# Performance work log

Hardware: AMD Instinct MI355X
Metric: run time of the kernel (lower is better)

The kernel has to match this reference:

```python
import jax, jax.numpy as jnp
import numpy as np

B, S, D, H = 2, 2048, 1024, 16
HD = D // H
NEG = -9000000000000000.0


def setup_inputs() -> dict:
    key = jax.random.key(0)
    ks = jax.random.split(key, 12)
    scale = 1.0 / np.sqrt(D)
    inp = {
        "k": jax.random.normal(ks[0], (B, S, D), jnp.float32),
        "q": jax.random.normal(ks[1], (B, S, D), jnp.float32),
        "v": jax.random.normal(ks[2], (B, S, D), jnp.float32),
        # causal mask, float (0/1), shape [B, 1, S, S] as expected by __call__
        "mask": jnp.broadcast_to(jnp.tril(jnp.ones((S, S), jnp.float32))[None, None], (B, 1, S, S)),
        "Wq": jax.random.normal(ks[3], (D, D), jnp.float32) * scale,
        "bq": jnp.zeros((D,), jnp.float32),
        "Wk": jax.random.normal(ks[4], (D, D), jnp.float32) * scale,
        "bk": jnp.zeros((D,), jnp.float32),
        "Wv": jax.random.normal(ks[5], (D, D), jnp.float32) * scale,
        "bv": jnp.zeros((D,), jnp.float32),
        "Wo": jax.random.normal(ks[6], (D, D), jnp.float32) * scale,
        "bo": jnp.zeros((D,), jnp.float32),
    }
    return inp


def _split_heads(x):
    # [B, S, D] -> [B, H, S, HD]
    return x.reshape(B, S, H, HD).transpose(0, 2, 1, 3)


def reference(k, q, v, mask, Wq, bq, Wk, bk, Wv, bv, Wo, bo):
    keys = _split_heads(k @ Wk + bk)
    queries = _split_heads(q @ Wq + bq)
    values = _split_heads(v @ Wv + bv)
    # scaled dot product with materialized scores (faithful to source)
    logits = jnp.einsum("bhqd,bhkd->bhqk", queries, keys) / np.sqrt(HD)
    logits = jnp.where(mask == 0, NEG, logits)
    attention = jax.nn.softmax(logits, axis=-1)
    out = jnp.einsum("bhqk,bhkd->bhqd", attention, values)
    out = out.transpose(0, 2, 1, 3).reshape(B, S, D)
    o = out @ Wo + bo
    return (o, attention)
```

## Files before the change

kernel.cpp:

```cpp
#include <hip/hip_runtime.h>
#include <stdint.h>

typedef unsigned short u16;
typedef short short8 __attribute__((ext_vector_type(8)));
typedef unsigned short ushort8 __attribute__((ext_vector_type(8)));
typedef float f32x4 __attribute__((ext_vector_type(4)));

#define S_LEN 2048
#define D_DIM 1024
#define H_NUM 16
#define HD_DIM 64
#define NEGBIG (-1e30f)

__device__ __forceinline__ float bf2f(u16 u) {
  union { uint32_t i; float f; } x; x.i = ((uint32_t)u) << 16; return x.f;
}
__device__ __forceinline__ u16 f2bf(float f) {
  union { float f; uint32_t i; } x; x.f = f;
  uint32_t u = x.i;
  uint32_t r = (u + 0x7fffu + ((u >> 16) & 1u)) >> 16;
  return (u16)r;
}
__device__ __forceinline__ f32x4 mfma16(short8 a, short8 b, f32x4 c) {
  return __builtin_amdgcn_mfma_f32_16x16x32_bf16(a, b, c, 0, 0, 0);
}
__device__ __forceinline__ bool mask_is_f32(const void* mask) {
  return *(const float*)mask == 1.0f;
}
__device__ __forceinline__ void async_cp16(const u16* g, u16* l) {
  __builtin_amdgcn_global_load_lds((const __attribute__((address_space(1))) unsigned int*)g,
                                   (__attribute__((address_space(3))) unsigned int*)l,
                                   16, 0, 0);
}

__global__ __launch_bounds__(256) void conv_qkv(const void* __restrict__ q,
                                                const void* __restrict__ k,
                                                const void* __restrict__ v,
                                                u16* __restrict__ out,
                                                const void* __restrict__ mask) {
  bool isf32 = mask_is_f32(mask);
  int z = blockIdx.y;
  const void* src = (z == 0) ? q : (z == 1) ? k : v;
  size_t i = ((size_t)blockIdx.x * 256 + threadIdx.x) * 8;
  u16* dst = out + (size_t)z * 4194304;
  if (isf32) {
    const f32x4* p = (const f32x4*)((const float*)src + i);
    f32x4 a = p[0], b = p[1];
    ushort8 o;
#pragma unroll
    for (int j = 0; j < 4; j++) { o[j] = f2bf(a[j]); o[4 + j] = f2bf(b[j]); }
    *(ushort8*)(dst + i) = o;
  } else {
    *(ushort8*)(dst + i) = *(const ushort8*)((const u16*)src + i);
  }
}

__global__ __launch_bounds__(256) void wtrans(const void* __restrict__ w0,
                                              const void* __restrict__ w1,
                                              const void* __restrict__ w2,
                                              const void* __restrict__ w3,
                                              u16* __restrict__ dstBase,
                                              const void* __restrict__ mask) {
  bool isf32 = mask_is_f32(mask);
  int y = blockIdx.y;
  const void* W = (y == 0) ? w0 : (y == 1) ? w1 : (y == 2) ? w2 : w3;
  u16* out = dstBase + (size_t)y * 1048576;
  __shared__ u16 t[64][65];
  int tile = blockIdx.x;
  int r0 = (tile >> 4) * 64, c0 = (tile & 15) * 64;
  int tid = threadIdx.x;
  int rr = tid >> 6, cc = tid & 63;
#pragma unroll
  for (int i = 0; i < 16; i++) {
    int r = i * 4 + rr;
    size_t idx = (size_t)(r0 + r) * 1024 + c0 + cc;
    t[r][cc] = isf32 ? f2bf(((const float*)W)[idx]) : ((const u16*)W)[idx];
  }
  __syncthreads();
#pragma unroll
  for (int i = 0; i < 16; i++) {
    int r = i * 4 + rr;
    out[(size_t)(c0 + r) * 1024 + r0 + cc] = t[cc][r];
  }
}

__global__ __launch_bounds__(256) void conv_bias(const void* __restrict__ b0,
                                                 const void* __restrict__ b1,
                                                 const void* __restrict__ b2,
                                                 const void* __restrict__ b3,
                                                 float* __restrict__ out,
                                                 const void* __restrict__ mask) {
  bool isf32 = mask_is_f32(mask);
  int y = blockIdx.y;
  const void* b = (y == 0) ? b0 : (y == 1) ? b1 : (y == 2) ? b2 : b3;
  int i = blockIdx.x * 256 + threadIdx.x;
  float v = isf32 ? ((const float*)b)[i] : bf2f(((const u16*)b)[i]);
  out[y * 1024 + i] = v;
}

__global__ __launch_bounds__(256) void v_transpose(const u16* __restrict__ V,
                                                   u16* __restrict__ Vt) {
  __shared__ u16 t[64][65];
  int bh = blockIdx.x, st = blockIdx.y;
  int b = bh >> 4, h = bh & 15;
  int tid = threadIdx.x;
  int rr = tid >> 6, cc = tid & 63;
#pragma unroll
  for (int i = 0; i < 16; i++) {
    int r = i * 4 + rr;
    t[r][cc] = V[(size_t)(b * S_LEN + st * 64 + r) * D_DIM + h * HD_DIM + cc];
  }
  __syncthreads();
#pragma unroll
  for (int i = 0; i < 16; i++) {
    int r = i * 4 + rr;
    Vt[(size_t)(bh * HD_DIM + r) * S_LEN + st * 64 + cc] = t[cc][r];
  }
}

__device__ __forceinline__ void gemm_body(const u16* __restrict__ A,
                                          const u16* __restrict__ Bt,
                                          const float* __restrict__ bias,
                                          void* __restrict__ C, bool cf32,
                                          int M, int N, int K, int m0, int n0) {
  __shared__ __align__(16) u16 lA[2][128 * 32];
  __shared__ __align__(16) u16 lB[2][128 * 32];
  int tid = threadIdx.x;
  int lane = tid & 63, w = tid >> 6;
  int wr = w >> 1, wc = w & 1;
  f32x4 acc[4][4] = {};
  const int nk = K >> 5;
  int grow = lane >> 2, gcol = (lane & 3) * 8;

#define GEMM_ISSUE(kt, buf)                                                              \
  {                                                                                      \
    _Pragma("unroll") for (int p = 0; p < 2; p++) {                                      \
      async_cp16(A + (size_t)(m0 + p * 64 + w * 16 + grow) * K + (kt) * 32 + gcol,       \
                 &lA[buf][p * 2048 + w * 512]);                                          \
      async_cp16(Bt + (size_t)(n0 + p * 64 + w * 16 + grow) * K + (kt) * 32 + gcol,      \
                 &lB[buf][p * 2048 + w * 512]);                                          \
    }                                                                                    \
  }

  GEMM_ISSUE(0, 0);
  __syncthreads();
  int cur = 0;
  for (int kt = 0; kt < nk; kt++) {
    if (kt + 1 < nk) GEMM_ISSUE(kt + 1, cur ^ 1);
    short8 af[4], bf[4];
#pragma unroll
    for (int i = 0; i < 4; i++) {
      af[i] = *(const short8*)(&lA[cur][(wr * 64 + i * 16 + (lane & 15)) * 32 + (lane >> 4) * 8]);
      bf[i] = *(const short8*)(&lB[cur][(wc * 64 + i * 16 + (lane & 15)) * 32 + (lane >> 4) * 8]);
    }
#pragma unroll
    for (int i = 0; i < 4; i++)
#pragma unroll
      for (int j = 0; j < 4; j++)
        acc[i][j] = mfma16(af[i], bf[j], acc[i][j]);
    __syncthreads();
    cur ^= 1;
  }
#undef GEMM_ISSUE
#pragma unroll
  for (int j = 0; j < 4; j++) {
    float bv = bias[n0 + wc * 64 + j * 16 + (lane & 15)];
#pragma unroll
    for (int i = 0; i < 4; i++) {
#pragma unroll
      for (int jj = 0; jj < 4; jj++) {
        int row = m0 + wr * 64 + i * 16 + ((lane >> 4) << 2) + jj;
        int col = n0 + wc * 64 + j * 16 + (lane & 15);
        float val = acc[i][j][jj] + bv;
        if (cf32) ((float*)C)[(size_t)row * N + col] = val;
        else ((u16*)C)[(size_t)row * N + col] = f2bf(val);
      }
    }
  }
}

__global__ __launch_bounds__(256, 2) void qkv_gemm(const u16* __restrict__ Ab,
                                                   const u16* __restrict__ WTall,
                                                   const float* __restrict__ biasF,
                                                   u16* __restrict__ outbase) {
  int z = blockIdx.z;
  gemm_body(Ab + (size_t)z * 4194304, WTall + (size_t)z * 1048576, biasF + z * 1024,
            outbase + (size_t)z * 4194304, false,
            4096, 1024, 1024, blockIdx.y * 128, blockIdx.x * 128);
}

__global__ __launch_bounds__(256, 2) void gemm_bt(const u16* __restrict__ A,
                                                  const u16* __restrict__ Bt,
                                                  const float* __restrict__ bias,
                                                  void* __restrict__ dout,
                                                  const void* __restrict__ mask) {
  bool isf32 = mask_is_f32(mask);
  gemm_body(A, Bt, bias, dout, isf32,
            4096, 1024, 1024, blockIdx.y * 128, blockIdx.x * 128);
}

__global__ __launch_bounds__(256, 2) void attn_fused(const u16* __restrict__ Qg,
                                                     const u16* __restrict__ Kg,
                                                     const u16* __restrict__ VtG,
                                                     void* __restrict__ dout,
                                                     u16* __restrict__ ctx,
                                                     const void* __restrict__ mask) {
  bool isf32 = mask_is_f32(mask);
  int x = blockIdx.x, bh = blockIdx.y;
  int b = bh >> 4, h = bh & 15;
  int tid = threadIdx.x, lane = tid & 63, w = tid >> 6;
  __shared__ __align__(16) u16 lK[2][64 * 72];
  __shared__ __align__(16) u16 lV[2][64 * 72];
  __shared__ __align__(16) u16 lP[64 * 72];

  float* attnF = (float*)dout + 4194304;
  u16* attnB = (u16*)dout + 4194304;
  int sr = tid >> 3, sc8 = (tid & 7) * 8;

  for (int s = 0; s < 2; s++) {
    int qt = (s == 0) ? x : 31 - x;
    int q0 = qt * 64;
    int nkv = qt + 1;

    short8 qf[2];
#pragma unroll
    for (int ks = 0; ks < 2; ks++)
      qf[ks] = *(const short8*)(Qg + (size_t)(b * S_LEN + q0 + w * 16 + (lane & 15)) * D_DIM +
                                h * HD_DIM + ks * 32 + (lane >> 4) * 8);

    ushort8 kreg[2], vreg[2];
    auto loadK = [&](int kt) {
#pragma unroll
      for (int p = 0; p < 2; p++)
        kreg[p] = *(const ushort8*)(Kg + (size_t)(b * S_LEN + kt * 64 + p * 32 + sr) * D_DIM +
                                    h * HD_DIM + sc8);
    };
    auto writeK = [&](int buf) {
#pragma unroll
      for (int p = 0; p < 2; p++)
        *(ushort8*)(&lK[buf][(p * 32 + sr) * 72 + sc8]) = kreg[p];
    };
    auto loadV = [&](int kt) {
#pragma unroll
      for (int p = 0; p < 2; p++)
        vreg[p] = *(const ushort8*)(VtG + (size_t)(bh * HD_DIM + p * 32 + sr) * S_LEN +
                                    kt * 64 + sc8);
    };
    auto writeV = [&](int buf) {
#pragma unroll
      for (int p = 0; p < 2; p++)
        *(ushort8*)(&lV[buf][(p * 32 + sr) * 72 + sc8]) = vreg[p];
    };
    auto computeS = [&](int buf, int kt, f32x4 (&sacc)[4]) {
      short8 bfr[4][2];
#pragma unroll
      for (int j = 0; j < 4; j++)
#pragma unroll
        for (int ks = 0; ks < 2; ks++)
          bfr[j][ks] = *(const short8*)(&lK[buf][(j * 16 + (lane & 15)) * 72 + ks * 32 + (lane >> 4) * 8]);
#pragma unroll
      for (int j = 0; j < 4; j++) {
        f32x4 a = {0.f, 0.f, 0.f, 0.f};
        a = mfma16(qf[0], bfr[j][0], a);
        a = mfma16(qf[1], bfr[j][1], a);
        sacc[j] = a;
      }
      bool needmask = (kt == qt);
#pragma unroll
      for (int j = 0; j < 4; j++)
#pragma unroll
        for (int jj = 0; jj < 4; jj++) {
          float sv = sacc[j][jj] * 0.125f;
          if (needmask) {
            int row = q0 + w * 16 + ((lane >> 4) << 2) + jj;
            int col = kt * 64 + j * 16 + (lane & 15);
            if (col > row) sv = NEGBIG;
          }
          sacc[j][jj] = sv;
        }
    };

    float m_[4], l_[4];
#pragma unroll
    for (int jj = 0; jj < 4; jj++) { m_[jj] = NEGBIG; l_[jj] = 0.f; }

    loadK(0); writeK(0);
    __syncthreads();
    int cur = 0;
    for (int kt = 0; kt < nkv; kt++) {
      if (kt + 1 < nkv) loadK(kt + 1);
      f32x4 sacc[4];
      computeS(cur, kt, sacc);
#pragma unroll
      for (int jj = 0; jj < 4; jj++) {
        float vm = fmaxf(fmaxf(sacc[0][jj], sacc[1][jj]),
                         fmaxf(sacc[2][jj], sacc[3][jj]));
        vm = fmaxf(vm, __shfl_xor(vm, 1));
        vm = fmaxf(vm, __shfl_xor(vm, 2));
        vm = fmaxf(vm, __shfl_xor(vm, 4));
        vm = fmaxf(vm, __shfl_xor(vm, 8));
        float nm = fmaxf(m_[jj], vm);
        float ss = __expf(sacc[0][jj] - nm) + __expf(sacc[1][jj] - nm) +
                   __expf(sacc[2][jj] - nm) + __expf(sacc[3][jj] - nm);
        ss += __shfl_xor(ss, 1);
        ss += __shfl_xor(ss, 2);
        ss += __shfl_xor(ss, 4);
        ss += __shfl_xor(ss, 8);
        l_[jj] = l_[jj] * __expf(m_[jj] - nm) + ss;
        m_[jj] = nm;
      }
      if (kt + 1 < nkv) writeK(cur ^ 1);
      __syncthreads();
      cur ^= 1;
    }
    float invl[4];
#pragma unroll
    for (int jj = 0; jj < 4; jj++) invl[jj] = 1.f / l_[jj];

    f32x4 oacc[4] = {};

    loadK(0); loadV(0); writeK(0); writeV(0);
    __syncthreads();
    cur = 0;
    for (int kt = 0; kt < nkv; kt++) {
      if (kt + 1 < nkv) { loadK(kt + 1); loadV(kt + 1); }
      f32x4 sacc[4];
      computeS(cur, kt, sacc);
#pragma unroll
      for (int j = 0; j < 4; j++)
#pragma unroll
        for (int jj = 0; jj < 4; jj++) {
          float p = __expf(sacc[j][jj] - m_[jj]) * invl[jj];
          int row = q0 + w * 16 + ((lane >> 4) << 2) + jj;
          int col = kt * 64 + j * 16 + (lane & 15);
          if (isf32) attnF[((size_t)bh * S_LEN + row) * S_LEN + col] = p;
          else attnB[((size_t)bh * S_LEN + row) * S_LEN + col] = f2bf(p);
          lP[(w * 16 + ((lane >> 4) << 2) + jj) * 72 + j * 16 + (lane & 15)] = f2bf(p);
        }
      short8 pa[2], vb[4][2];
#pragma unroll
      for (int ks = 0; ks < 2; ks++)
        pa[ks] = *(const short8*)(&lP[(w * 16 + (lane & 15)) * 72 + ks * 32 + (lane >> 4) * 8]);
#pragma unroll
      for (int f = 0; f < 4; f++)
#pragma unroll
        for (int ks = 0; ks < 2; ks++)
          vb[f][ks] = *(const short8*)(&lV[cur][(f * 16 + (lane & 15)) * 72 + ks * 32 + (lane >> 4) * 8]);
#pragma unroll
      for (int f = 0; f < 4; f++) {
        oacc[f] = mfma16(pa[0], vb[f][0], oacc[f]);
        oacc[f] = mfma16(pa[1], vb[f][1], oacc[f]);
      }
      if (kt + 1 < nkv) { writeK(cur ^ 1); writeV(cur ^ 1); }
      __syncthreads();
      cur ^= 1;
    }

    {
      int z0 = nkv * 64;
      if (isf32) {
        int zc4 = (S_LEN - z0) >> 2;
        if (zc4 > 0) {
          f32x4 zz = {0.f, 0.f, 0.f, 0.f};
          for (int r = tid >> 5; r < 64; r += 8)
            for (int c = tid & 31; c < zc4; c += 32)
              *(f32x4*)(attnF + ((size_t)bh * S_LEN + q0 + r) * S_LEN + z0 + c * 4) = zz;
        }
      } else {
        int zc8 = (S_LEN - z0) >> 3;
        if (zc8 > 0) {
          ushort8 zz = {0, 0, 0, 0, 0, 0, 0, 0};
          for (int r = tid >> 5; r < 64; r += 8)
            for (int c = tid & 31; c < zc8; c += 32)
              *(ushort8*)(attnB + ((size_t)bh * S_LEN + q0 + r) * S_LEN + z0 + c * 8) = zz;
        }
      }
    }

#pragma unroll
    for (int f = 0; f < 4; f++)
#pragma unroll
      for (int jj = 0; jj < 4; jj++) {
        int row = q0 + w * 16 + ((lane >> 4) << 2) + jj;
        int col = h * HD_DIM + f * 16 + (lane & 15);
        ctx[(size_t)(b * S_LEN + row) * D_DIM + col] = f2bf(oacc[f][jj]);
      }
  }
}

extern "C" void kernel_launch(void* const* d_in, const int* in_sizes, int n_in,
                              void* d_out, int out_size, void* d_ws, size_t ws_size,
                              hipStream_t stream) {
  const void* kin = d_in[0];
  const void* qin = d_in[1];
  const void* vin = d_in[2];
  const void* mask = d_in[3];
  const void* Wq = d_in[4];
  const void* bq = d_in[5];
  const void* Wk = d_in[6];
  const void* bk = d_in[7];
  const void* Wv = d_in[8];
  const void* bv = d_in[9];
  const void* Wo = d_in[10];
  const void* bo = d_in[11];

  u16* ws = (u16*)d_ws;
  u16* WT = ws;
  float* biasF = (float*)(ws + 4 * 1048576);
  u16* Cb = ws + 4 * 1048576 + 8192;
  u16* Qp = Cb + 3 * 4194304;
  u16* Kp = Qp + 4194304;
  u16* Vp = Kp + 4194304;
  u16* Vt = Vp + 4194304;
  u16* ctx = Vt + 4194304;

  conv_qkv<<<dim3(2048, 3), 256, 0, stream>>>(qin, kin, vin, Cb, mask);
  wtrans<<<dim3(256, 4), 256, 0, stream>>>(Wq, Wk, Wv, Wo, WT, mask);
  conv_bias<<<dim3(4, 4), 256, 0, stream>>>(bq, bk, bv, bo, biasF, mask);
  qkv_gemm<<<dim3(8, 32, 3), 256, 0, stream>>>(Cb, WT, biasF, Qp);
  v_transpose<<<dim3(32, 32), 256, 0, stream>>>(Vp, Vt);
  attn_fused<<<dim3(16, 32), 256, 0, stream>>>(Qp, Kp, Vt, d_out, ctx, mask);
  gemm_bt<<<dim3(8, 32), 256, 0, stream>>>(ctx, WT + 3 * 1048576, biasF + 3072, d_out, mask);
}
```

Baseline: 299.1 us.

## Compute transposed QK^T with K/V fragments loaded directly from global memory

```diff
diff --git a/kernel.cpp b/kernel.cpp
--- a/kernel.cpp
+++ b/kernel.cpp
@@ -4,6 +4,7 @@
 typedef unsigned short u16;
 typedef short short8 __attribute__((ext_vector_type(8)));
 typedef unsigned short ushort8 __attribute__((ext_vector_type(8)));
+typedef unsigned short us4 __attribute__((ext_vector_type(4)));
 typedef float f32x4 __attribute__((ext_vector_type(4)));
 
 #define S_LEN 2048
@@ -199,161 +200,146 @@
             4096, 1024, 1024, blockIdx.y * 128, blockIdx.x * 128);
 }
 
-__global__ __launch_bounds__(256, 2) void attn_fused(const u16* __restrict__ Qg,
-                                                     const u16* __restrict__ Kg,
-                                                     const u16* __restrict__ VtG,
-                                                     void* __restrict__ dout,
-                                                     u16* __restrict__ ctx,
-                                                     const void* __restrict__ mask) {
+__global__ __launch_bounds__(256) void attn_fused(const u16* __restrict__ Qg,
+                                                  const u16* __restrict__ Kg,
+                                                  const u16* __restrict__ VtG,
+                                                  void* __restrict__ dout,
+                                                  u16* __restrict__ ctx,
+                                                  const void* __restrict__ mask) {
   bool isf32 = mask_is_f32(mask);
   int x = blockIdx.x, bh = blockIdx.y;
   int b = bh >> 4, h = bh & 15;
   int tid = threadIdx.x, lane = tid & 63, w = tid >> 6;
-  __shared__ __align__(16) u16 lK[2][64 * 72];
-  __shared__ __align__(16) u16 lV[2][64 * 72];
-  __shared__ __align__(16) u16 lP[64 * 72];
-
+  __shared__ __align__(16) u16 lP[4][16 * 72];
   float* attnF = (float*)dout + 4194304;
   u16* attnB = (u16*)dout + 4194304;
-  int sr = tid >> 3, sc8 = (tid & 7) * 8;
+  u16* lPw = &lP[w][0];
 
   for (int s = 0; s < 2; s++) {
     int qt = (s == 0) ? x : 31 - x;
     int q0 = qt * 64;
     int nkv = qt + 1;
+    int qrow = q0 + w * 16 + (lane & 15);
 
     short8 qf[2];
 #pragma unroll
     for (int ks = 0; ks < 2; ks++)
-      qf[ks] = *(const short8*)(Qg + (size_t)(b * S_LEN + q0 + w * 16 + (lane & 15)) * D_DIM +
+      qf[ks] = *(const short8*)(Qg + (size_t)(b * S_LEN + qrow) * D_DIM +
                                 h * HD_DIM + ks * 32 + (lane >> 4) * 8);
 
-    ushort8 kreg[2], vreg[2];
-    auto loadK = [&](int kt) {
-#pragma unroll
-      for (int p = 0; p < 2; p++)
-        kreg[p] = *(const ushort8*)(Kg + (size_t)(b * S_LEN + kt * 64 + p * 32 + sr) * D_DIM +
-                                    h * HD_DIM + sc8);
+    short8 kfA[4][2], kfB[4][2];
+    auto loadKf = [&](short8 (&kf)[4][2], int kt) {
+#pragma unroll
+      for (int j = 0; j < 4; j++)
+#pragma unroll
+        for (int ks = 0; ks < 2; ks++)
+          kf[j][ks] = *(const short8*)(Kg + (size_t)(b * S_LEN + kt * 64 + j * 16 + (lane & 15)) * D_DIM +
+                                       h * HD_DIM + ks * 32 + (lane >> 4) * 8);
     };
-    auto writeK = [&](int buf) {
-#pragma unroll
-      for (int p = 0; p < 2; p++)
-        *(ushort8*)(&lK[buf][(p * 32 + sr) * 72 + sc8]) = kreg[p];
+    auto loadVb = [&](short8 (&vb)[4][2], int kt) {
+#pragma unroll
+      for (int f = 0; f < 4; f++)
+#pragma unroll
+        for (int ks = 0; ks < 2; ks++)
+          vb[f][ks] = *(const short8*)(VtG + (size_t)(bh * HD_DIM + f * 16 + (lane & 15)) * S_LEN +
+                                       kt * 64 + ks * 32 + (lane >> 4) * 8);
     };
-    auto loadV = [&](int kt) {
-#pragma unroll
-      for (int p = 0; p < 2; p++)
-        vreg[p] = *(const ushort8*)(VtG + (size_t)(bh * HD_DIM + p * 32 + sr) * S_LEN +
-                                    kt * 64 + sc8);
-    };
-    auto writeV = [&](int buf) {
-#pragma unroll
-      for (int p = 0; p < 2; p++)
-        *(ushort8*)(&lV[buf][(p * 32 + sr) * 72 + sc8]) = vreg[p];
-    };
-    auto computeS = [&](int buf, int kt, f32x4 (&sacc)[4]) {
-      short8 bfr[4][2];
-#pragma unroll
-      for (int j = 0; j < 4; j++)
-#pragma unroll
-        for (int ks = 0; ks < 2; ks++)
-          bfr[j][ks] = *(const short8*)(&lK[buf][(j * 16 + (lane & 15)) * 72 + ks * 32 + (lane >> 4) * 8]);
+    auto qkT = [&](short8 (&kf)[4][2], int kt, f32x4 (&sc)[4]) {
 #pragma unroll
       for (int j = 0; j < 4; j++) {
         f32x4 a = {0.f, 0.f, 0.f, 0.f};
-        a = mfma16(qf[0], bfr[j][0], a);
-        a = mfma16(qf[1], bfr[j][1], a);
-        sacc[j] = a;
+        a = mfma16(kf[j][0], qf[0], a);
+        a = mfma16(kf[j][1], qf[1], a);
+        sc[j] = a;
       }
       bool needmask = (kt == qt);
 #pragma unroll
       for (int j = 0; j < 4; j++)
 #pragma unroll
         for (int jj = 0; jj < 4; jj++) {
-          float sv = sacc[j][jj] * 0.125f;
+          float sv = sc[j][jj] * 0.125f;
           if (needmask) {
-            int row = q0 + w * 16 + ((lane >> 4) << 2) + jj;
-            int col = kt * 64 + j * 16 + (lane & 15);
-            if (col > row) sv = NEGBIG;
+            int kv = kt * 64 + j * 16 + ((lane >> 4) << 2) + jj;
+            if (kv > qrow) sv = NEGBIG;
           }
-          sacc[j][jj] = sv;
+          sc[j][jj] = sv;
         }
     };
 
-    float m_[4], l_[4];
-#pragma unroll
-    for (int jj = 0; jj < 4; jj++) { m_[jj] = NEGBIG; l_[jj] = 0.f; }
-
-    loadK(0); writeK(0);
-    __syncthreads();
-    int cur = 0;
-    for (int kt = 0; kt < nkv; kt++) {
-      if (kt + 1 < nkv) loadK(kt + 1);
-      f32x4 sacc[4];
-      computeS(cur, kt, sacc);
-#pragma unroll
-      for (int jj = 0; jj < 4; jj++) {
-        float vm = fmaxf(fmaxf(sacc[0][jj], sacc[1][jj]),
-                         fmaxf(sacc[2][jj], sacc[3][jj]));
-        vm = fmaxf(vm, __shfl_xor(vm, 1));
-        vm = fmaxf(vm, __shfl_xor(vm, 2));
-        vm = fmaxf(vm, __shfl_xor(vm, 4));
-        vm = fmaxf(vm, __shfl_xor(vm, 8));
-        float nm = fmaxf(m_[jj], vm);
-        float ss = __expf(sacc[0][jj] - nm) + __expf(sacc[1][jj] - nm) +
-                   __expf(sacc[2][jj] - nm) + __expf(sacc[3][jj] - nm);
-        ss += __shfl_xor(ss, 1);
-        ss += __shfl_xor(ss, 2);
-        ss += __shfl_xor(ss, 4);
-        ss += __shfl_xor(ss, 8);
-        l_[jj] = l_[jj] * __expf(m_[jj] - nm) + ss;
-        m_[jj] = nm;
-      }
-      if (kt + 1 < nkv) writeK(cur ^ 1);
-      __syncthreads();
-      cur ^= 1;
+    float m_ = NEGBIG, l_ = 0.f;
+    auto statTile = [&](short8 (&kf)[4][2], int kt) {
+      f32x4 sc[4];
+      qkT(kf, kt, sc);
+      float vm = sc[0][0];
+#pragma unroll
+      for (int j = 0; j < 4; j++)
+#pragma unroll
+        for (int jj = 0; jj < 4; jj++) vm = fmaxf(vm, sc[j][jj]);
+      vm = fmaxf(vm, __shfl_xor(vm, 16));
+      vm = fmaxf(vm, __shfl_xor(vm, 32));
+      float nm = fmaxf(m_, vm);
+      float ss = 0.f;
+#pragma unroll
+      for (int j = 0; j < 4; j++)
+#pragma unroll
+        for (int jj = 0; jj < 4; jj++) ss += __expf(sc[j][jj] - nm);
+      ss += __shfl_xor(ss, 16);
+      ss += __shfl_xor(ss, 32);
+      l_ = l_ * __expf(m_ - nm) + ss;
+      m_ = nm;
+    };
+
+    loadKf(kfA, 0);
+    for (int kt = 0; kt < nkv; kt += 2) {
+      if (kt + 1 < nkv) loadKf(kfB, kt + 1);
+      statTile(kfA, kt);
+      if (kt + 1 < nkv) {
+        if (kt + 2 < nkv) loadKf(kfA, kt + 2);
+        statTile(kfB, kt + 1);
+      }
     }
-    float invl[4];
-#pragma unroll
-    for (int jj = 0; jj < 4; jj++) invl[jj] = 1.f / l_[jj];
+    float invl = 1.f / l_;
 
     f32x4 oacc[4] = {};
-
-    loadK(0); loadV(0); writeK(0); writeV(0);
-    __syncthreads();
-    cur = 0;
-    for (int kt = 0; kt < nkv; kt++) {
-      if (kt + 1 < nkv) { loadK(kt + 1); loadV(kt + 1); }
-      f32x4 sacc[4];
-      computeS(cur, kt, sacc);
-#pragma unroll
-      for (int j = 0; j < 4; j++)
+    auto pvTile = [&](short8 (&kf)[4][2], short8 (&vb)[4][2], int kt) {
+      f32x4 sc[4];
+      qkT(kf, kt, sc);
+#pragma unroll
+      for (int j = 0; j < 4; j++) {
+        f32x4 p4;
+        us4 pb;
 #pragma unroll
         for (int jj = 0; jj < 4; jj++) {
-          float p = __expf(sacc[j][jj] - m_[jj]) * invl[jj];
-          int row = q0 + w * 16 + ((lane >> 4) << 2) + jj;
-          int col = kt * 64 + j * 16 + (lane & 15);
-          if (isf32) attnF[((size_t)bh * S_LEN + row) * S_LEN + col] = p;
-          else attnB[((size_t)bh * S_LEN + row) * S_LEN + col] = f2bf(p);
-          lP[(w * 16 + ((lane >> 4) << 2) + jj) * 72 + j * 16 + (lane & 15)] = f2bf(p);
+          p4[jj] = __expf(sc[j][jj] - m_) * invl;
+          pb[jj] = f2bf(p4[jj]);
         }
-      short8 pa[2], vb[4][2];
+        size_t goff = ((size_t)bh * S_LEN + qrow) * S_LEN + kt * 64 + j * 16 + ((lane >> 4) << 2);
+        if (isf32) *(f32x4*)(attnF + goff) = p4;
+        else *(us4*)(attnB + goff) = pb;
+        *(us4*)(&lPw[(lane & 15) * 72 + j * 16 + ((lane >> 4) << 2)]) = pb;
+      }
+      short8 pa[2];
 #pragma unroll
       for (int ks = 0; ks < 2; ks++)
-        pa[ks] = *(const short8*)(&lP[(w * 16 + (lane & 15)) * 72 + ks * 32 + (lane >> 4) * 8]);
-#pragma unroll
-      for (int f = 0; f < 4; f++)
-#pragma unroll
-        for (int ks = 0; ks < 2; ks++)
-          vb[f][ks] = *(const short8*)(&lV[cur][(f * 16 + (lane & 15)) * 72 + ks * 32 + (lane >> 4) * 8]);
+        pa[ks] = *(const short8*)(&lPw[(lane & 15) * 72 + ks * 32 + (lane >> 4) * 8]);
 #pragma unroll
       for (int f = 0; f < 4; f++) {
         oacc[f] = mfma16(pa[0], vb[f][0], oacc[f]);
         oacc[f] = mfma16(pa[1], vb[f][1], oacc[f]);
       }
-      if (kt + 1 < nkv) { writeK(cur ^ 1); writeV(cur ^ 1); }
-      __syncthreads();
-      cur ^= 1;
+    };
+
+    short8 vbR[4][2];
+    loadKf(kfA, 0);
+    for (int kt = 0; kt < nkv; kt += 2) {
+      loadVb(vbR, kt);
+      if (kt + 1 < nkv) loadKf(kfB, kt + 1);
+      pvTile(kfA, vbR, kt);
+      if (kt + 1 < nkv) {
+        loadVb(vbR, kt + 1);
+        if (kt + 2 < nkv) loadKf(kfA, kt + 2);
+        pvTile(kfB, vbR, kt + 1);
+      }
     }
 
     {
```

After: 366.2 us. 1.22x slower.
